# Performance work log

Measured on AMD Instinct MI355X. Metric: run time of the kernel, lower is better.

Reference implementation:

```python
import jax, jax.numpy as jnp
import numpy as np

B, V, H = 4, 256, 128
EPS = 1e-5


def setup_inputs() -> dict:
    key = jax.random.key(0)
    ks = jax.random.split(key, 16)
    s = 1.0 / np.sqrt(H)
    d = {}
    d["h"] = jax.random.normal(ks[0], (B, V, H), jnp.float32)
    d["e"] = jax.random.normal(ks[1], (B, V, V, H), jnp.float32)
    d["A"] = jax.random.bernoulli(ks[2], 0.5, (B, V, V))
    d["S"] = jax.random.bernoulli(ks[3], 0.5, (B, V, V))
    for i, n in enumerate("UVABC"):
        d["W" + n] = (jax.random.normal(ks[4 + i], (H, H), jnp.float32) * s)
        d["b" + n] = jnp.zeros((H,), jnp.float32)
    d["gamma_h"] = jnp.ones((H,), jnp.float32)
    d["beta_h"] = jnp.zeros((H,), jnp.float32)
    d["gamma_e"] = jnp.ones((H,), jnp.float32)
    d["beta_e"] = jnp.zeros((H,), jnp.float32)
    return d


def _batchnorm(x2d, gamma, beta):
    # BatchNorm1d with batch statistics (track_running_stats=False), biased var
    m = x2d.mean(axis=0)
    v = x2d.var(axis=0)
    return (x2d - m) * jax.lax.rsqrt(v + EPS) * gamma + beta


def reference(h, e, A, S, WU, bU, WV, bV, WA, bA, WB, bB, WC, bC,
              gamma_h, beta_h, gamma_e, beta_e):
    b, v, hd = h.shape
    h_in, e_in = h, e

    Uh = h @ WU.T + bU                      # (B,V,H)
    Vh = h @ WV.T + bV                      # (B,V,H)
    Ah = h @ WA.T + bA
    Bh = h @ WB.T + bB
    Ce = e @ WC.T + bC                      # (B,V,V,H)

    # e_new[b,i,j] = Ah[b,j] + Bh[b,i] + Ce[b,i,j]
    e_new = Ah[:, None, :, :] + Bh[:, :, None, :] + Ce
    gates = jax.nn.sigmoid(e_new)

    # aggregate(Vh, S, gates): zero where S is True, then sum over j
    Vh_b = Vh[:, None, :, :]                # (B,1,V,H) -> neighbor j features
    agg_S = jnp.sum(jnp.where(S[..., None], 0.0, gates * Vh_b), axis=2)
    # aggregate(Vh, A, gates=1): sum_j (1 - A[i,j]) * Vh[j] as a matmul
    agg_A = jnp.einsum('bij,bjh->bih', (~A).astype(Vh.dtype), Vh)

    h_new = Uh + agg_S + agg_A

    h_new = _batchnorm(h_new.reshape(b * v, hd), gamma_h, beta_h).reshape(b, v, hd)
    e_new = _batchnorm(e_new.reshape(b * v * v, hd), gamma_e, beta_e).reshape(b, v, v, hd)

    h_out = h_in + jax.nn.relu(h_new)
    e_out = e_in + jax.nn.relu(e_new)
    return (h_out, e_out)
```

## Files before the change

### kernel.cpp

```cpp
#include <hip/hip_runtime.h>

#define BB 4
#define VV 256
#define HH 128
#define NROWS (BB*VV)
#define NE_CNT (BB*VV*VV)
#define EPSV 1e-5f

typedef float4 f4;

__device__ __forceinline__ float sigm(float x) {
    return 1.f / (1.f + __expf(-x));
}

__global__ __launch_bounds__(256) void k_linear4(
    const float* __restrict__ h,
    const float* __restrict__ W0, const float* __restrict__ b0,
    const float* __restrict__ W1, const float* __restrict__ b1,
    const float* __restrict__ W2, const float* __restrict__ b2,
    const float* __restrict__ W3, const float* __restrict__ b3,
    float* __restrict__ out)
{
    __shared__ float hs[4*HH];
    const int tid = threadIdx.x;
    const int r0  = blockIdx.x * 4;
    if (tid < 128) {
        int r = tid >> 5, kq = (tid & 31) << 2;
        *(f4*)&hs[r*HH + kq] = *(const f4*)&h[(r0 + r)*HH + kq];
    }
    __syncthreads();
    const int n  = tid & 127;
    const int s0 = tid >> 7;
    const float* Ws[4] = {W0, W1, W2, W3};
    const float* bs[4] = {b0, b1, b2, b3};
    for (int ss = 0; ss < 2; ++ss) {
        const int sel = s0 + ss*2;
        const float* wrow = Ws[sel] + n*HH;
        float a0=0.f, a1=0.f, a2=0.f, a3=0.f;
        for (int kq = 0; kq < 32; ++kq) {
            f4 w = *(const f4*)&wrow[kq<<2];
            float wq[4] = {w.x, w.y, w.z, w.w};
            #pragma unroll
            for (int q = 0; q < 4; ++q) {
                int k = (kq<<2) + q;
                float wv = wq[q];
                a0 += hs[0*HH + k] * wv;
                a1 += hs[1*HH + k] * wv;
                a2 += hs[2*HH + k] * wv;
                a3 += hs[3*HH + k] * wv;
            }
        }
        float bias = bs[sel][n];
        float* o = out + sel*(NROWS*HH);
        o[(r0+0)*HH + n] = a0 + bias;
        o[(r0+1)*HH + n] = a1 + bias;
        o[(r0+2)*HH + n] = a2 + bias;
        o[(r0+3)*HH + n] = a3 + bias;
    }
}

__global__ __launch_bounds__(256) void k_transpose(
    const float* __restrict__ in, float* __restrict__ out)
{
    __shared__ float t[32][33];
    int ti = blockIdx.x >> 2, tj = blockIdx.x & 3;
    int tx = threadIdx.x & 31, ty = threadIdx.x >> 5;
    for (int yy = ty; yy < 32; yy += 8)
        t[yy][tx] = in[(ti*32 + yy)*HH + tj*32 + tx];
    __syncthreads();
    for (int yy = ty; yy < 32; yy += 8)
        out[(tj*32 + yy)*HH + ti*32 + tx] = t[tx][yy];
}

__global__ __launch_bounds__(256, 2) void k_edge(
    const float* __restrict__ e, const int* __restrict__ A, const int* __restrict__ S,
    const float* __restrict__ WCt, const float* __restrict__ bC,
    const float* __restrict__ Ahw, const float* __restrict__ Bhw,
    const float* __restrict__ Vhw,
    float* __restrict__ eout, float* __restrict__ aggS, float* __restrict__ aggA,
    float* __restrict__ sums)
{
    __shared__ float es[256*36];
    __shared__ float wc[32*132];
    __shared__ float s_aggS[HH], s_aggA[HH], s_sum[HH], s_ssq[HH];

    const int t  = threadIdx.x;
    const int bi = blockIdx.x;
    const int b  = bi >> 8;
    if (t < HH) { s_aggS[t]=0.f; s_aggA[t]=0.f; s_sum[t]=0.f; s_ssq[t]=0.f; }

    const int tn  = t & 7;
    const int tjg = t >> 3;

    float acc[8][16];
    #pragma unroll
    for (int jj = 0; jj < 8; ++jj)
        #pragma unroll
        for (int q = 0; q < 16; ++q) acc[jj][q] = 0.f;

    const f4* e4   = (const f4*)e;
    const f4* wct4 = (const f4*)WCt;

    for (int kc = 0; kc < 4; ++kc) {
        __syncthreads();
        #pragma unroll
        for (int m = 0; m < 8; ++m) {
            int idx = m*256 + t;
            int j = idx >> 3, kq = idx & 7;
            *(f4*)&es[j*36 + kq*4] = e4[(bi*VV + j)*32 + kc*8 + kq];
        }
        #pragma unroll
        for (int m = 0; m < 4; ++m) {
            int idx = m*256 + t;
            int k = idx >> 5, n4 = idx & 31;
            *(f4*)&wc[k*132 + n4*4] = wct4[(kc*32 + k)*32 + n4];
        }
        __syncthreads();
        #pragma unroll
        for (int kq = 0; kq < 8; ++kq) {
            f4 aj[8];
            #pragma unroll
            for (int jj = 0; jj < 8; ++jj)
                aj[jj] = *(const f4*)&es[(tjg + jj*32)*36 + kq*4];
            #pragma unroll
            for (int kk = 0; kk < 4; ++kk) {
                f4 wq[4];
                #pragma unroll
                for (int q = 0; q < 4; ++q)
                    wq[q] = *(const f4*)&wc[(kq*4 + kk)*132 + tn*4 + q*32];
                #pragma unroll
                for (int jj = 0; jj < 8; ++jj) {
                    float a = (kk==0) ? aj[jj].x : (kk==1) ? aj[jj].y
                            : (kk==2) ? aj[jj].z : aj[jj].w;
                    #pragma unroll
                    for (int q = 0; q < 4; ++q) {
                        acc[jj][q*4+0] += a*wq[q].x;
                        acc[jj][q*4+1] += a*wq[q].y;
                        acc[jj][q*4+2] += a*wq[q].z;
                        acc[jj][q*4+3] += a*wq[q].w;
                    }
                }
            }
        }
    }

    float bcv[16], bhv[16];
    #pragma unroll
    for (int q = 0; q < 4; ++q) {
        f4 bc4 = *(const f4*)&bC[tn*4 + q*32];
        f4 bh4 = *(const f4*)&Bhw[bi*HH + tn*4 + q*32];
        bcv[q*4+0]=bc4.x; bcv[q*4+1]=bc4.y; bcv[q*4+2]=bc4.z; bcv[q*4+3]=bc4.w;
        bhv[q*4+0]=bh4.x; bhv[q*4+1]=bh4.y; bhv[q*4+2]=bh4.z; bhv[q*4+3]=bh4.w;
    }
    float sm[16], sq[16], aS[16], aA[16];
    #pragma unroll
    for (int q = 0; q < 16; ++q) { sm[q]=0.f; sq[q]=0.f; aS[q]=0.f; aA[q]=0.f; }

    const int* Sp = S + bi*VV;
    const int* Ap = A + bi*VV;
    #pragma unroll
    for (int jj = 0; jj < 8; ++jj) {
        const int j = tjg + jj*32;
        const float* ahp = &Ahw[(b*VV + j)*HH];
        const float* vhp = &Vhw[(b*VV + j)*HH];
        const int Sij = Sp[j], Aij = Ap[j];
        #pragma unroll
        for (int q = 0; q < 4; ++q) {
            f4 ah = *(const f4*)&ahp[tn*4 + q*32];
            f4 vh = *(const f4*)&vhp[tn*4 + q*32];
            f4 env;
            env.x = acc[jj][q*4+0] + bcv[q*4+0] + bhv[q*4+0] + ah.x;
            env.y = acc[jj][q*4+1] + bcv[q*4+1] + bhv[q*4+1] + ah.y;
            env.z = acc[jj][q*4+2] + bcv[q*4+2] + bhv[q*4+2] + ah.z;
            env.w = acc[jj][q*4+3] + bcv[q*4+3] + bhv[q*4+3] + ah.w;
            *(f4*)&eout[((size_t)(bi*VV) + j)*HH + tn*4 + q*32] = env;
            float vv[4] = {vh.x, vh.y, vh.z, vh.w};
            float ev[4] = {env.x, env.y, env.z, env.w};
            #pragma unroll
            for (int qq = 0; qq < 4; ++qq) {
                float v = ev[qq];
                sm[q*4+qq] += v;
                sq[q*4+qq] += v*v;
                if (!Aij) aA[q*4+qq] += vv[qq];
                if (!Sij) aS[q*4+qq] += vv[qq] * sigm(v);
            }
        }
    }
    #pragma unroll
    for (int q = 0; q < 4; ++q)
        #pragma unroll
        for (int qq = 0; qq < 4; ++qq) {
            int n = tn*4 + q*32 + qq;
            atomicAdd(&s_sum[n],  sm[q*4+qq]);
            atomicAdd(&s_ssq[n],  sq[q*4+qq]);
            atomicAdd(&s_aggS[n], aS[q*4+qq]);
            atomicAdd(&s_aggA[n], aA[q*4+qq]);
        }
    __syncthreads();
    if (t < HH) {
        aggS[bi*HH + t] = s_aggS[t];
        aggA[bi*HH + t] = s_aggA[t];
        atomicAdd(&sums[t],      s_sum[t]);
        atomicAdd(&sums[HH + t], s_ssq[t]);
    }
}

__global__ __launch_bounds__(256) void k_hnew(
    const float* __restrict__ Uh, const float* __restrict__ aggS,
    const float* __restrict__ aggA, float* __restrict__ h_new,
    float* __restrict__ sums)
{
    __shared__ float ssm[HH], ssq[HH];
    const int tid = threadIdx.x;
    if (tid < 128) { ssm[tid]=0.f; ssq[tid]=0.f; }
    __syncthreads();
    int gid = blockIdx.x*256 + tid;
    f4 u = *(const f4*)&Uh[gid*4];
    f4 s = *(const f4*)&aggS[gid*4];
    f4 a = *(const f4*)&aggA[gid*4];
    float v0=u.x+s.x+a.x, v1=u.y+s.y+a.y, v2=u.z+s.z+a.z, v3=u.w+s.w+a.w;
    *(f4*)&h_new[gid*4] = make_float4(v0,v1,v2,v3);
    int n0 = (gid*4) & 127;
    atomicAdd(&ssm[n0+0], v0); atomicAdd(&ssq[n0+0], v0*v0);
    atomicAdd(&ssm[n0+1], v1); atomicAdd(&ssq[n0+1], v1*v1);
    atomicAdd(&ssm[n0+2], v2); atomicAdd(&ssq[n0+2], v2*v2);
    atomicAdd(&ssm[n0+3], v3); atomicAdd(&ssq[n0+3], v3*v3);
    __syncthreads();
    if (tid < 128) {
        atomicAdd(&sums[256 + tid], ssm[tid]);
        atomicAdd(&sums[384 + tid], ssq[tid]);
    }
}

__global__ void k_stats(const float* __restrict__ sums, float* __restrict__ outs,
                        const float* __restrict__ gamma_e, const float* __restrict__ beta_e,
                        const float* __restrict__ gamma_h, const float* __restrict__ beta_h)
{
    int n = threadIdx.x;
    float em  = sums[n] * (1.f/(float)NE_CNT);
    float ev  = sums[128+n] * (1.f/(float)NE_CNT) - em*em;
    float esc = rsqrtf(ev + EPSV) * gamma_e[n];
    outs[n]       = esc;
    outs[128 + n] = beta_e[n] - em*esc;
    float hm  = sums[256+n] * (1.f/1024.f);
    float hv  = sums[384+n] * (1.f/1024.f) - hm*hm;
    float hsc = rsqrtf(hv + EPSV) * gamma_h[n];
    outs[256 + n] = hsc;
    outs[384 + n] = beta_h[n] - hm*hsc;
}

__global__ __launch_bounds__(256) void k_hout(
    const float* __restrict__ h_in, const float* __restrict__ h_new,
    const float* __restrict__ outs, float* __restrict__ hout)
{
    int gid = blockIdx.x*256 + threadIdx.x;
    int n0 = (gid*4) & 127;
    f4 x  = *(const f4*)&h_new[gid*4];
    f4 hi = *(const f4*)&h_in[gid*4];
    f4 sc = *(const f4*)&outs[256 + n0];
    f4 sh = *(const f4*)&outs[384 + n0];
    f4 y;
    y.x = fmaxf(x.x*sc.x + sh.x, 0.f) + hi.x;
    y.y = fmaxf(x.y*sc.y + sh.y, 0.f) + hi.y;
    y.z = fmaxf(x.z*sc.z + sh.z, 0.f) + hi.z;
    y.w = fmaxf(x.w*sc.w + sh.w, 0.f) + hi.w;
    *(f4*)&hout[gid*4] = y;
}

__global__ __launch_bounds__(256) void k_eout(
    const float* __restrict__ e_in, const float* __restrict__ outs,
    float* __restrict__ eio)
{
    size_t gid = (size_t)blockIdx.x*256 + threadIdx.x;
    int n0 = ((int)(gid & 31)) << 2;
    f4 x  = *(const f4*)&eio[gid*4];
    f4 ei = *(const f4*)&e_in[gid*4];
    f4 sc = *(const f4*)&outs[n0];
    f4 sh = *(const f4*)&outs[128 + n0];
    f4 y;
    y.x = fmaxf(x.x*sc.x + sh.x, 0.f) + ei.x;
    y.y = fmaxf(x.y*sc.y + sh.y, 0.f) + ei.y;
    y.z = fmaxf(x.z*sc.z + sh.z, 0.f) + ei.z;
    y.w = fmaxf(x.w*sc.w + sh.w, 0.f) + ei.w;
    *(f4*)&eio[gid*4] = y;
}

extern "C" void kernel_launch(void* const* d_in, const int* in_sizes, int n_in,
                              void* d_out, int out_size, void* d_ws, size_t ws_size,
                              hipStream_t stream)
{
    (void)in_sizes; (void)n_in; (void)out_size; (void)ws_size;
    const float* h   = (const float*)d_in[0];
    const float* e   = (const float*)d_in[1];
    const int*   A   = (const int*)d_in[2];
    const int*   S   = (const int*)d_in[3];
    const float* WU  = (const float*)d_in[4];   const float* bU = (const float*)d_in[5];
    const float* WV  = (const float*)d_in[6];   const float* bV = (const float*)d_in[7];
    const float* WA_ = (const float*)d_in[8];   const float* bA = (const float*)d_in[9];
    const float* WB_ = (const float*)d_in[10];  const float* bB = (const float*)d_in[11];
    const float* WC_ = (const float*)d_in[12];  const float* bC = (const float*)d_in[13];
    const float* gamma_h = (const float*)d_in[14]; const float* beta_h = (const float*)d_in[15];
    const float* gamma_e = (const float*)d_in[16]; const float* beta_e = (const float*)d_in[17];

    float* ws    = (float*)d_ws;
    float* Uh    = ws;
    float* Vh    = ws + 131072;
    float* Ahw   = ws + 262144;
    float* Bhw   = ws + 393216;
    float* aggS  = ws + 524288;
    float* aggA  = ws + 655360;
    float* h_new = ws + 786432;
    float* WCt   = ws + 917504;
    float* sums  = ws + 933888;
    float* outs  = ws + 934400;

    float* hout = (float*)d_out;
    float* eout = (float*)d_out + NROWS*HH;

    hipMemsetAsync(sums, 0, 512*sizeof(float), stream);
    k_linear4 <<<256,   256, 0, stream>>>(h, WU,bU, WV,bV, WA_,bA, WB_,bB, Uh);
    k_transpose<<<16,   256, 0, stream>>>(WC_, WCt);
    k_edge    <<<1024,  256, 0, stream>>>(e, A, S, WCt, bC, Ahw, Bhw, Vh,
                                          eout, aggS, aggA, sums);
    k_hnew    <<<128,   256, 0, stream>>>(Uh, aggS, aggA, h_new, sums);
    k_stats   <<<1,     128, 0, stream>>>(sums, outs, gamma_e, beta_e, gamma_h, beta_h);
    k_hout    <<<128,   256, 0, stream>>>(h, h_new, outs, hout);
    k_eout    <<<32768, 256, 0, stream>>>(e, outs, eout);
}
```

Baseline: 546.9 us.

## Use split-bf16 MFMA for node and edge linear projections

Replaces the FP32 scalar GEMMs in the node linear and edge kernels with bf16 MFMA 16x16x32 instructions. To keep accuracy close to fp32, each operand is split into hi and lo bf16 parts and three MFMAs are summed per tile. A new prep kernel pre-packs all five weight matrices into fragment layout, which replaces the transpose kernel. The edge kernel drops its LDS staging of e and weights, loads A fragments directly from global memory, and reduces statistics with wave shuffles before the shared atomics. The split-bf16 trick still loses a little precision compared with fp32, and the direct global loads may be less coalesced.

```diff
diff --git a/kernel.cpp b/kernel.cpp
--- a/kernel.cpp
+++ b/kernel.cpp
@@ -8,194 +8,210 @@
 #define EPSV 1e-5f
 
 typedef float4 f4;
+typedef short bf16x8 __attribute__((ext_vector_type(8)));
+typedef float f32x4 __attribute__((ext_vector_type(4)));
 
 __device__ __forceinline__ float sigm(float x) {
     return 1.f / (1.f + __expf(-x));
 }
 
-__global__ __launch_bounds__(256) void k_linear4(
+__device__ __forceinline__ unsigned short bf16_rne(float x) {
+    union { float f; unsigned u; } v; v.f = x;
+    unsigned r = v.u + 0x7fffu + ((v.u >> 16) & 1u);
+    return (unsigned short)(r >> 16);
+}
+__device__ __forceinline__ float bf16_to_f(unsigned short h) {
+    union { unsigned u; float f; } v; v.u = ((unsigned)h) << 16;
+    return v.f;
+}
+__device__ __forceinline__ void split_bf16(float x, short& hi, short& lo) {
+    unsigned short h = bf16_rne(x);
+    hi = (short)h;
+    lo = (short)bf16_rne(x - bf16_to_f(h));
+}
+
+__device__ __forceinline__ f32x4 mfma16(bf16x8 a, bf16x8 b, f32x4 c) {
+    return __builtin_amdgcn_mfma_f32_16x16x32_bf16(a, b, c, 0, 0, 0);
+}
+
+__global__ __launch_bounds__(256) void k_prep(
+    const float* __restrict__ W0, const float* __restrict__ W1,
+    const float* __restrict__ W2, const float* __restrict__ W3,
+    const float* __restrict__ W4,
+    short* __restrict__ WFH, short* __restrict__ WFL)
+{
+    int g = blockIdx.x*256 + threadIdx.x;
+    if (g >= 5*2048) return;
+    int mat  = g >> 11;
+    int rem  = g & 2047;
+    int f    = rem >> 6;
+    int lane = rem & 63;
+    int nt = f >> 2, kt = f & 3;
+    const float* Ws[5] = {W0,W1,W2,W3,W4};
+    const float* src = Ws[mat] + (nt*16 + (lane & 15))*HH + kt*32 + (lane>>4)*8;
+    f4 a0 = *(const f4*)&src[0];
+    f4 a1 = *(const f4*)&src[4];
+    float av[8] = {a0.x,a0.y,a0.z,a0.w,a1.x,a1.y,a1.z,a1.w};
+    bf16x8 hv, lv;
+    #pragma unroll
+    for (int j = 0; j < 8; ++j) { short hh, ll; split_bf16(av[j], hh, ll); hv[j]=hh; lv[j]=ll; }
+    size_t o = ((size_t)(mat*32 + f)*64 + lane);
+    ((bf16x8*)WFH)[o] = hv;
+    ((bf16x8*)WFL)[o] = lv;
+}
+
+__global__ __launch_bounds__(256, 2) void k_lin(
     const float* __restrict__ h,
-    const float* __restrict__ W0, const float* __restrict__ b0,
-    const float* __restrict__ W1, const float* __restrict__ b1,
-    const float* __restrict__ W2, const float* __restrict__ b2,
-    const float* __restrict__ W3, const float* __restrict__ b3,
+    const short* __restrict__ WFH, const short* __restrict__ WFL,
+    const float* __restrict__ b0, const float* __restrict__ b1,
+    const float* __restrict__ b2, const float* __restrict__ b3,
     float* __restrict__ out)
 {
-    __shared__ float hs[4*HH];
-    const int tid = threadIdx.x;
-    const int r0  = blockIdx.x * 4;
-    if (tid < 128) {
-        int r = tid >> 5, kq = (tid & 31) << 2;
-        *(f4*)&hs[r*HH + kq] = *(const f4*)&h[(r0 + r)*HH + kq];
-    }
-    __syncthreads();
-    const int n  = tid & 127;
-    const int s0 = tid >> 7;
-    const float* Ws[4] = {W0, W1, W2, W3};
-    const float* bs[4] = {b0, b1, b2, b3};
-    for (int ss = 0; ss < 2; ++ss) {
-        const int sel = s0 + ss*2;
-        const float* wrow = Ws[sel] + n*HH;
-        float a0=0.f, a1=0.f, a2=0.f, a3=0.f;
-        for (int kq = 0; kq < 32; ++kq) {
-            f4 w = *(const f4*)&wrow[kq<<2];
-            float wq[4] = {w.x, w.y, w.z, w.w};
-            #pragma unroll
-            for (int q = 0; q < 4; ++q) {
-                int k = (kq<<2) + q;
-                float wv = wq[q];
-                a0 += hs[0*HH + k] * wv;
-                a1 += hs[1*HH + k] * wv;
-                a2 += hs[2*HH + k] * wv;
-                a3 += hs[3*HH + k] * wv;
-            }
-        }
-        float bias = bs[sel][n];
-        float* o = out + sel*(NROWS*HH);
-        o[(r0+0)*HH + n] = a0 + bias;
-        o[(r0+1)*HH + n] = a1 + bias;
-        o[(r0+2)*HH + n] = a2 + bias;
-        o[(r0+3)*HH + n] = a3 + bias;
-    }
-}
-
-__global__ __launch_bounds__(256) void k_transpose(
-    const float* __restrict__ in, float* __restrict__ out)
-{
-    __shared__ float t[32][33];
-    int ti = blockIdx.x >> 2, tj = blockIdx.x & 3;
-    int tx = threadIdx.x & 31, ty = threadIdx.x >> 5;
-    for (int yy = ty; yy < 32; yy += 8)
-        t[yy][tx] = in[(ti*32 + yy)*HH + tj*32 + tx];
-    __syncthreads();
-    for (int yy = ty; yy < 32; yy += 8)
-        out[(tj*32 + yy)*HH + ti*32 + tx] = t[tx][yy];
+    const int t = threadIdx.x;
+    const int lane = t & 63, w = t >> 6;
+    const int jt = blockIdx.x;
+    const int m = lane & 15, quad = lane >> 4, nl = m;
+
+    bf16x8 Ahi[4], Alo[4];
+    const float* arow = h + (jt*16 + m)*HH + quad*8;
+    #pragma unroll
+    for (int kt = 0; kt < 4; ++kt) {
+        f4 a0 = *(const f4*)&arow[kt*32];
+        f4 a1 = *(const f4*)&arow[kt*32 + 4];
+        float av[8] = {a0.x,a0.y,a0.z,a0.w,a1.x,a1.y,a1.z,a1.w};
+        bf16x8 hv, lv;
+        #pragma unroll
+        for (int j = 0; j < 8; ++j) { short hh,ll; split_bf16(av[j],hh,ll); hv[j]=hh; lv[j]=ll; }
+        Ahi[kt]=hv; Alo[kt]=lv;
+    }
+    const bf16x8* BH = (const bf16x8*)WFH + (size_t)w*32*64;
+    const bf16x8* BL = (const bf16x8*)WFL + (size_t)w*32*64;
+
+    f32x4 acc[8];
+    #pragma unroll
+    for (int nt = 0; nt < 8; ++nt) acc[nt] = (f32x4){0.f,0.f,0.f,0.f};
+    #pragma unroll
+    for (int nt = 0; nt < 8; ++nt)
+        #pragma unroll
+        for (int kt = 0; kt < 4; ++kt) {
+            bf16x8 bh = BH[(nt*4+kt)*64 + lane];
+            bf16x8 bl = BL[(nt*4+kt)*64 + lane];
+            acc[nt] = mfma16(Ahi[kt], bh, acc[nt]);
+            acc[nt] = mfma16(Alo[kt], bh, acc[nt]);
+            acc[nt] = mfma16(Ahi[kt], bl, acc[nt]);
+        }
+
+    const float* bias = (w==0)?b0:(w==1)?b1:(w==2)?b2:b3;
+    float* o = out + (size_t)w*(NROWS*HH);
+    #pragma unroll
+    for (int nt = 0; nt < 8; ++nt) {
+        const int n = nt*16 + nl;
+        const float bv = bias[n];
+        #pragma unroll
+        for (int r = 0; r < 4; ++r) {
+            const int j = jt*16 + quad*4 + r;
+            o[j*HH + n] = acc[nt][r] + bv;
+        }
+    }
 }
 
 __global__ __launch_bounds__(256, 2) void k_edge(
     const float* __restrict__ e, const int* __restrict__ A, const int* __restrict__ S,
-    const float* __restrict__ WCt, const float* __restrict__ bC,
+    const short* __restrict__ WFH, const short* __restrict__ WFL,
+    const float* __restrict__ bC,
     const float* __restrict__ Ahw, const float* __restrict__ Bhw,
     const float* __restrict__ Vhw,
     float* __restrict__ eout, float* __restrict__ aggS, float* __restrict__ aggA,
     float* __restrict__ sums)
 {
-    __shared__ float es[256*36];
-    __shared__ float wc[32*132];
     __shared__ float s_aggS[HH], s_aggA[HH], s_sum[HH], s_ssq[HH];
-
-    const int t  = threadIdx.x;
-    const int bi = blockIdx.x;
-    const int b  = bi >> 8;
+    const int t = threadIdx.x;
+    const int bi = blockIdx.x, b = bi >> 8;
+    const int lane = t & 63, w = t >> 6;
+    const int nl = lane & 15, quad = lane >> 4;
     if (t < HH) { s_aggS[t]=0.f; s_aggA[t]=0.f; s_sum[t]=0.f; s_ssq[t]=0.f; }
-
-    const int tn  = t & 7;
-    const int tjg = t >> 3;
-
-    float acc[8][16];
-    #pragma unroll
-    for (int jj = 0; jj < 8; ++jj)
-        #pragma unroll
-        for (int q = 0; q < 16; ++q) acc[jj][q] = 0.f;
-
-    const f4* e4   = (const f4*)e;
-    const f4* wct4 = (const f4*)WCt;
-
-    for (int kc = 0; kc < 4; ++kc) {
-        __syncthreads();
-        #pragma unroll
-        for (int m = 0; m < 8; ++m) {
-            int idx = m*256 + t;
-            int j = idx >> 3, kq = idx & 7;
-            *(f4*)&es[j*36 + kq*4] = e4[(bi*VV + j)*32 + kc*8 + kq];
-        }
-        #pragma unroll
-        for (int m = 0; m < 4; ++m) {
-            int idx = m*256 + t;
-            int k = idx >> 5, n4 = idx & 31;
-            *(f4*)&wc[k*132 + n4*4] = wct4[(kc*32 + k)*32 + n4];
-        }
-        __syncthreads();
-        #pragma unroll
-        for (int kq = 0; kq < 8; ++kq) {
-            f4 aj[8];
+    __syncthreads();
+
+    float bcv[8], bhv[8];
+    #pragma unroll
+    for (int nt = 0; nt < 8; ++nt) {
+        bcv[nt] = bC[nt*16 + nl];
+        bhv[nt] = Bhw[bi*HH + nt*16 + nl];
+    }
+    float sm[8], sq[8], aS[8], aA[8];
+    #pragma unroll
+    for (int nt = 0; nt < 8; ++nt) { sm[nt]=0.f; sq[nt]=0.f; aS[nt]=0.f; aA[nt]=0.f; }
+
+    const bf16x8* BH = (const bf16x8*)WFH + (size_t)4*32*64;
+    const bf16x8* BL = (const bf16x8*)WFL + (size_t)4*32*64;
+
+    for (int jt = 0; jt < 4; ++jt) {
+        const int jtg = w*4 + jt;
+        bf16x8 Ahi[4], Alo[4];
+        const float* arow = e + ((size_t)bi*VV + jtg*16 + nl)*HH + quad*8;
+        #pragma unroll
+        for (int kt = 0; kt < 4; ++kt) {
+            f4 a0 = *(const f4*)&arow[kt*32];
+            f4 a1 = *(const f4*)&arow[kt*32 + 4];
+            float av[8] = {a0.x,a0.y,a0.z,a0.w,a1.x,a1.y,a1.z,a1.w};
+            bf16x8 hv, lv;
             #pragma unroll
-            for (int jj = 0; jj < 8; ++jj)
-                aj[jj] = *(const f4*)&es[(tjg + jj*32)*36 + kq*4];
+            for (int j = 0; j < 8; ++j) { short hh,ll; split_bf16(av[j],hh,ll); hv[j]=hh; lv[j]=ll; }
+            Ahi[kt]=hv; Alo[kt]=lv;
+        }
+        f32x4 acc[8];
+        #pragma unroll
+        for (int nt = 0; nt < 8; ++nt) acc[nt] = (f32x4){0.f,0.f,0.f,0.f};
+        #pragma unroll
+        for (int nt = 0; nt < 8; ++nt)
             #pragma unroll
-            for (int kk = 0; kk < 4; ++kk) {
-                f4 wq[4];
-                #pragma unroll
-                for (int q = 0; q < 4; ++q)
-                    wq[q] = *(const f4*)&wc[(kq*4 + kk)*132 + tn*4 + q*32];
-                #pragma unroll
-                for (int jj = 0; jj < 8; ++jj) {
-                    float a = (kk==0) ? aj[jj].x : (kk==1) ? aj[jj].y
-                            : (kk==2) ? aj[jj].z : aj[jj].w;
-                    #pragma unroll
-                    for (int q = 0; q < 4; ++q) {
-                        acc[jj][q*4+0] += a*wq[q].x;
-                        acc[jj][q*4+1] += a*wq[q].y;
-                        acc[jj][q*4+2] += a*wq[q].z;
-                        acc[jj][q*4+3] += a*wq[q].w;
-                    }
-                }
+            for (int kt = 0; kt < 4; ++kt) {
+                bf16x8 bh = BH[(nt*4+kt)*64 + lane];
+                bf16x8 bl = BL[(nt*4+kt)*64 + lane];
+                acc[nt] = mfma16(Ahi[kt], bh, acc[nt]);
+                acc[nt] = mfma16(Alo[kt], bh, acc[nt]);
+                acc[nt] = mfma16(Ahi[kt], bl, acc[nt]);
             }
-        }
-    }
-
-    float bcv[16], bhv[16];
-    #pragma unroll
-    for (int q = 0; q < 4; ++q) {
-        f4 bc4 = *(const f4*)&bC[tn*4 + q*32];
-        f4 bh4 = *(const f4*)&Bhw[bi*HH + tn*4 + q*32];
-        bcv[q*4+0]=bc4.x; bcv[q*4+1]=bc4.y; bcv[q*4+2]=bc4.z; bcv[q*4+3]=bc4.w;
-        bhv[q*4+0]=bh4.x; bhv[q*4+1]=bh4.y; bhv[q*4+2]=bh4.z; bhv[q*4+3]=bh4.w;
-    }
-    float sm[16], sq[16], aS[16], aA[16];
-    #pragma unroll
-    for (int q = 0; q < 16; ++q) { sm[q]=0.f; sq[q]=0.f; aS[q]=0.f; aA[q]=0.f; }
-
-    const int* Sp = S + bi*VV;
-    const int* Ap = A + bi*VV;
-    #pragma unroll
-    for (int jj = 0; jj < 8; ++jj) {
-        const int j = tjg + jj*32;
-        const float* ahp = &Ahw[(b*VV + j)*HH];
-        const float* vhp = &Vhw[(b*VV + j)*HH];
-        const int Sij = Sp[j], Aij = Ap[j];
-        #pragma unroll
-        for (int q = 0; q < 4; ++q) {
-            f4 ah = *(const f4*)&ahp[tn*4 + q*32];
-            f4 vh = *(const f4*)&vhp[tn*4 + q*32];
-            f4 env;
-            env.x = acc[jj][q*4+0] + bcv[q*4+0] + bhv[q*4+0] + ah.x;
-            env.y = acc[jj][q*4+1] + bcv[q*4+1] + bhv[q*4+1] + ah.y;
-            env.z = acc[jj][q*4+2] + bcv[q*4+2] + bhv[q*4+2] + ah.z;
-            env.w = acc[jj][q*4+3] + bcv[q*4+3] + bhv[q*4+3] + ah.w;
-            *(f4*)&eout[((size_t)(bi*VV) + j)*HH + tn*4 + q*32] = env;
-            float vv[4] = {vh.x, vh.y, vh.z, vh.w};
-            float ev[4] = {env.x, env.y, env.z, env.w};
+        const int j0 = jtg*16 + quad*4;
+        #pragma unroll
+        for (int r = 0; r < 4; ++r) {
+            const int j = j0 + r;
+            const int Sij = S[bi*VV + j];
+            const int Aij = A[bi*VV + j];
+            const float* ahp = Ahw + ((size_t)b*VV + j)*HH;
+            const float* vhp = Vhw + ((size_t)b*VV + j)*HH;
+            float* eo = eout + ((size_t)bi*VV + j)*HH;
             #pragma unroll
-            for (int qq = 0; qq < 4; ++qq) {
-                float v = ev[qq];
-                sm[q*4+qq] += v;
-                sq[q*4+qq] += v*v;
-                if (!Aij) aA[q*4+qq] += vv[qq];
-                if (!Sij) aS[q*4+qq] += vv[qq] * sigm(v);
+            for (int nt = 0; nt < 8; ++nt) {
+                const int n = nt*16 + nl;
+                float env = acc[nt][r] + bcv[nt] + bhv[nt] + ahp[n];
+                eo[n] = env;
+                float vh = vhp[n];
+                sm[nt] += env;
+                sq[nt] += env*env;
+                if (!Aij) aA[nt] += vh;
+                if (!Sij) aS[nt] += vh * sigm(env);
             }
         }
     }
     #pragma unroll
-    for (int q = 0; q < 4; ++q)
-        #pragma unroll
-        for (int qq = 0; qq < 4; ++qq) {
-            int n = tn*4 + q*32 + qq;
-            atomicAdd(&s_sum[n],  sm[q*4+qq]);
-            atomicAdd(&s_ssq[n],  sq[q*4+qq]);
-            atomicAdd(&s_aggS[n], aS[q*4+qq]);
-            atomicAdd(&s_aggA[n], aA[q*4+qq]);
-        }
+    for (int nt = 0; nt < 8; ++nt) {
+        float v;
+        v = sm[nt]; v += __shfl_xor(v,16,64); v += __shfl_xor(v,32,64); sm[nt]=v;
+        v = sq[nt]; v += __shfl_xor(v,16,64); v += __shfl_xor(v,32,64); sq[nt]=v;
+        v = aS[nt]; v += __shfl_xor(v,16,64); v += __shfl_xor(v,32,64); aS[nt]=v;
+        v = aA[nt]; v += __shfl_xor(v,16,64); v += __shfl_xor(v,32,64); aA[nt]=v;
+    }
+    if (quad == 0) {
+        #pragma unroll
+        for (int nt = 0; nt < 8; ++nt) {
+            const int n = nt*16 + nl;
+            atomicAdd(&s_sum[n],  sm[nt]);
+            atomicAdd(&s_ssq[n],  sq[nt]);
+            atomicAdd(&s_aggS[n], aS[nt]);
+            atomicAdd(&s_aggA[n], aA[nt]);
+        }
+    }
     __syncthreads();
     if (t < HH) {
         aggS[bi*HH + t] = s_aggS[t];
@@ -310,20 +326,21 @@
     float* aggS  = ws + 524288;
     float* aggA  = ws + 655360;
     float* h_new = ws + 786432;
-    float* WCt   = ws + 917504;
-    float* sums  = ws + 933888;
-    float* outs  = ws + 934400;
+    float* sums  = ws + 917504;
+    float* outs  = ws + 918016;
+    short* WFH = (short*)(ws + 786432);
+    short* WFL = (short*)(ws + 786432 + 40960);
 
     float* hout = (float*)d_out;
     float* eout = (float*)d_out + NROWS*HH;
 
     hipMemsetAsync(sums, 0, 512*sizeof(float), stream);
-    k_linear4 <<<256,   256, 0, stream>>>(h, WU,bU, WV,bV, WA_,bA, WB_,bB, Uh);
-    k_transpose<<<16,   256, 0, stream>>>(WC_, WCt);
-    k_edge    <<<1024,  256, 0, stream>>>(e, A, S, WCt, bC, Ahw, Bhw, Vh,
-                                          eout, aggS, aggA, sums);
-    k_hnew    <<<128,   256, 0, stream>>>(Uh, aggS, aggA, h_new, sums);
-    k_stats   <<<1,     128, 0, stream>>>(sums, outs, gamma_e, beta_e, gamma_h, beta_h);
-    k_hout    <<<128,   256, 0, stream>>>(h, h_new, outs, hout);
-    k_eout    <<<32768, 256, 0, stream>>>(e, outs, eout);
-}
+    k_prep <<<40,    256, 0, stream>>>(WU, WV, WA_, WB_, WC_, WFH, WFL);
+    k_lin  <<<64,    256, 0, stream>>>(h, WFH, WFL, bU, bV, bA, bB, Uh);
+    k_edge <<<1024,  256, 0, stream>>>(e, A, S, WFH, WFL, bC, Ahw, Bhw, Vh,
+                                       eout, aggS, aggA, sums);
+    k_hnew <<<128,   256, 0, stream>>>(Uh, aggS, aggA, h_new, sums);
+    k_stats<<<1,     128, 0, stream>>>(sums, outs, gamma_e, beta_e, gamma_h, beta_h);
+    k_hout <<<128,   256, 0, stream>>>(h, h_new, outs, hout);
+    k_eout <<<32768, 256, 0, stream>>>(e, outs, eout);
+}
```

Result: slower. 563.5 us (+3.0%).
